# Performance work log

Hardware: AMD Instinct MI355X
Metric: run time of the kernel (lower is better)

Reference implementation:

```python
import jax, jax.numpy as jnp
import numpy as np

R, C, B, E, H = 16, 256, 12, 768, 12  # rows, cols, batch(==heads, see notes), embed, heads
D = E // H
NUM_BUCKETS, MAX_DISTANCE = 32, 50000


def _relative_position_bucket(distances):
    # T5-style log-spaced buckets, matching the torch code (trunc toward zero).
    n = jnp.abs(distances)
    max_exact = NUM_BUCKETS // 2
    is_small = n < max_exact
    nf = jnp.maximum(n.astype(jnp.float32), 1.0)  # guard log(0); masked by is_small
    val_large = max_exact + (
        jnp.log(nf / max_exact) / np.log(MAX_DISTANCE / max_exact) * (NUM_BUCKETS - max_exact - 1)
    ).astype(jnp.int32)
    val_large = jnp.minimum(val_large, NUM_BUCKETS - 1)
    return jnp.where(is_small, n.astype(jnp.int32), val_large)


def setup_inputs() -> dict:
    key = jax.random.key(0)
    ks = jax.random.split(key, 11)
    s = 1.0 / np.sqrt(E)
    x = jax.random.normal(ks[0], (R, C, B, E), jnp.float32)
    distances = jax.random.randint(ks[1], (B, C, C), 0, MAX_DISTANCE, jnp.int32)
    Wq = jax.random.normal(ks[2], (E, E), jnp.float32) * s
    bq = jnp.zeros((E,), jnp.float32)
    Wk = jax.random.normal(ks[3], (E, E), jnp.float32) * s
    bk = jnp.zeros((E,), jnp.float32)
    Wv = jax.random.normal(ks[4], (E, E), jnp.float32) * s
    bv = jnp.zeros((E,), jnp.float32)
    Wo = jax.random.normal(ks[5], (E, E), jnp.float32) * s
    bo = jnp.zeros((E,), jnp.float32)
    rel_bias = jax.random.normal(ks[6], (NUM_BUCKETS, H), jnp.float32) * 0.02
    return dict(x=x, distances=distances, Wq=Wq, bq=bq, Wk=Wk, bk=bk,
                Wv=Wv, bv=bv, Wo=Wo, bo=bo, rel_bias=rel_bias)


def reference(x, distances, Wq, bq, Wk, bk, Wv, bv, Wo, bo, rel_bias):
    scaling = (D ** -0.5) / np.sqrt(R)  # align_scaling: head_dim^-0.5 / sqrt(num_rows)
    q = (x @ Wq.T + bq).reshape(R, C, B, H, D) * scaling
    k = (x @ Wk.T + bk).reshape(R, C, B, H, D)
    # row-aggregated scores: sum over rows r -> (h, n, i, j)
    attn = jnp.einsum('rinhd,rjnhd->hnij', q, k)
    # relative position bias: (n, i, j) -> buckets -> (n, i, j, h) -> (n, h, i, j)
    buckets = _relative_position_bucket(distances)
    bias = jnp.transpose(rel_bias[buckets], (0, 3, 1, 2))
    # NOTE: source adds (n,h,i,j) bias onto (h,n,i,j) scores positionally; valid since B == H.
    attn = attn + bias
    probs = jax.nn.softmax(attn, axis=-1)  # (h, n, i, j)
    v = (x @ Wv.T + bv).reshape(R, C, B, H, D)
    ctx = jnp.einsum('hnij,rjnhd->rinhd', probs, v).reshape(R, C, B, E)
    out = ctx @ Wo.T + bo
    return out, probs
```

## Files before the change

kernel.cpp:

```cpp
#include <hip/hip_runtime.h>
#include <stdint.h>
#include <math.h>

#define R_ 16
#define C_ 256
#define B_ 12
#define E_ 768
#define H_ 12
#define D_ 64
#define TOK (R_*C_*B_)
#define HALF_TOK 24576

#define VT_N_ELEMS 3145728
#define CTX_N_ELEMS 3145728
#define QK_HALF 37748736

typedef __bf16 bf16x8 __attribute__((ext_vector_type(8)));
typedef float floatx4 __attribute__((ext_vector_type(4)));

__device__ __forceinline__ unsigned short f2bf(float f) {
    union { unsigned int i; float f; } v; v.f = f;
    unsigned int i = v.i;
    return (unsigned short)((i + 0x7fffu + ((i >> 16) & 1u)) >> 16);
}
__device__ __forceinline__ bf16x8 cvt8(floatx4 lo, floatx4 hi) {
    bf16x8 r;
    r[0] = (__bf16)lo[0]; r[1] = (__bf16)lo[1]; r[2] = (__bf16)lo[2]; r[3] = (__bf16)lo[3];
    r[4] = (__bf16)hi[0]; r[5] = (__bf16)hi[1]; r[6] = (__bf16)hi[2]; r[7] = (__bf16)hi[3];
    return r;
}
__device__ __forceinline__ void gload16(const unsigned short* g, unsigned short* l) {
    __builtin_amdgcn_global_load_lds(
        (const __attribute__((address_space(1))) unsigned int*)g,
        (__attribute__((address_space(3))) unsigned int*)l, 16, 0, 0);
}

template<int MODE>
__device__ __forceinline__ void gemm_body(const void* __restrict__ Ap,
                                          const void* __restrict__ Btp,
                                          const float* __restrict__ bias,
                                          void* __restrict__ Cout,
                                          int nBase, int rbx, int rby, int rbz,
                                          unsigned short* As, unsigned short* Bs)
{
    constexpr bool AGL = (MODE == 0 || MODE == 1 || MODE == 4);
    constexpr int K = (MODE == 1) ? 1024 : ((MODE == 2) ? 256 : 768);
    constexpr int kIters = K >> 5;
    constexpr int GX = (MODE==0) ? 12 : (MODE==1) ? 2 : (MODE==2) ? 8 : 6;
    constexpr int GY = (MODE==0) ? 192 : (MODE==1) ? 2 : (MODE==2) ? 2 : 32;
    constexpr int GZ = (MODE==0) ? 1 : (MODE==1) ? 144 : (MODE==2) ? 24 : 2;

    const int tid  = threadIdx.x;
    const int wave = tid >> 6, lane = tid & 63;
    const int quad = lane >> 4, l15 = lane & 15;
    const int wr = wave >> 1, wc = wave & 1;

    const int lin = (rbz * GY + rby) * GX + rbx;
    const int tt  = (lin & 7) * ((GX * GY * GZ) >> 3) + (lin >> 3);
    const int bx  = tt % GX;
    const int rem = tt / GX;
    const int by  = rem % GY, bz = rem / GY;
    const int row0 = by * 128, col0 = bx * 128;

    int hIdx = 0, nn = 0, nIdx = 0;
    if (MODE == 1) { hIdx = bz % 12; nIdx = bz / 12; }
    if (MODE == 2) { hIdx = bz % 12; nn = bz / 12; nIdx = nBase + nn; }
    if (MODE == 3 || MODE == 4) { nn = bz; nIdx = nBase + nn; }

    const int rA0 = tid >> 2;
    const int ck  = tid & 3;
    const int sw  = (tid >> 3) & 3;
    const int kko = ((ck ^ sw) << 3);

    const unsigned short* Bt = (const unsigned short*)Btp;
    const unsigned short *gB0, *gB1;
    if (MODE == 1) {
        gB0 = Bt + ((size_t)bz * 256 + col0 + rA0) * 1024 + kko;
        gB1 = Bt + ((size_t)bz * 256 + col0 + rA0 + 64) * 1024 + kko;
    } else if (MODE == 2) {
        gB0 = Bt + (((size_t)nn * 12 + hIdx) * 1024 + col0 + rA0) * 256 + kko;
        gB1 = Bt + (((size_t)nn * 12 + hIdx) * 1024 + col0 + rA0 + 64) * 256 + kko;
    } else {
        gB0 = Bt + (size_t)(col0 + rA0) * 768 + kko;
        gB1 = Bt + (size_t)(col0 + rA0 + 64) * 768 + kko;
    }

    const unsigned short* gA0u = nullptr; const unsigned short* gA1u = nullptr;
    const float* gA0f = nullptr; const float* gA1f = nullptr;
    if (MODE == 0) {
        gA0u = (const unsigned short*)Ap + (size_t)(row0 + rA0) * 768 + kko;
        gA1u = (const unsigned short*)Ap + (size_t)(row0 + rA0 + 64) * 768 + kko;
    } else if (MODE == 1) {
        gA0u = (const unsigned short*)Ap + ((size_t)bz * 256 + row0 + rA0) * 1024 + kko;
        gA1u = (const unsigned short*)Ap + ((size_t)bz * 256 + row0 + rA0 + 64) * 1024 + kko;
    } else if (MODE == 4) {
        gA0u = (const unsigned short*)Ap + (size_t)nn * CTX_N_ELEMS
               + (size_t)(row0 + rA0) * 768 + kko;
        gA1u = (const unsigned short*)Ap + (size_t)nn * CTX_N_ELEMS
               + (size_t)(row0 + rA0 + 64) * 768 + kko;
    } else if (MODE == 3) {
        gA0f = (const float*)Ap + ((size_t)(row0 + rA0) * 12 + nIdx) * 768 + kko;
        gA1f = (const float*)Ap + ((size_t)(row0 + rA0 + 64) * 12 + nIdx) * 768 + kko;
    } else {
        gA0f = (const float*)Ap + ((size_t)(hIdx * 12 + nIdx)) * 65536
               + (size_t)(row0 + rA0) * 256 + kko;
        gA1f = (const float*)Ap + ((size_t)(hIdx * 12 + nIdx)) * 65536
               + (size_t)(row0 + rA0 + 64) * 256 + kko;
    }

    unsigned short* lA0 = As + wave * 512;
    unsigned short* lA1 = As + 2048 + wave * 512;
    unsigned short* lB0 = Bs + wave * 512;
    unsigned short* lB1 = Bs + 2048 + wave * 512;

    const floatx4 zero = {0.f, 0.f, 0.f, 0.f};
    floatx4 acc[4][4];
#pragma unroll
    for (int i = 0; i < 4; ++i)
#pragma unroll
        for (int j = 0; j < 4; ++j) acc[i][j] = zero;

    const int chO = ((quad ^ ((l15 >> 1) & 3)) << 3);

    floatx4 u0l = zero, u0h = zero, u1l = zero, u1h = zero;
    floatx4 p0l = zero, p0h = zero, p1l = zero, p1h = zero;
    if (!AGL) {
        u0l = *(const floatx4*)(gA0f);     u0h = *(const floatx4*)(gA0f + 4);
        u1l = *(const floatx4*)(gA1f);     u1h = *(const floatx4*)(gA1f + 4);
    }

#define GSTEP(KT, UL0, UH0, UL1, UH1, PL0, PH0, PL1, PH1)                         \
    {                                                                              \
        __syncthreads();                                \
        gload16(gB0 + (KT) * 32, lB0);                                             \
        gload16(gB1 + (KT) * 32, lB1);                                             \
        if (AGL) {                                                                 \
            gload16(gA0u + (KT) * 32, lA0);                                        \
            gload16(gA1u + (KT) * 32, lA1);                                        \
        } else {                                                                   \
            *(bf16x8*)(As + tid * 8)        = cvt8(UL0, UH0);                      \
            *(bf16x8*)(As + 2048 + tid * 8) = cvt8(UL1, UH1);                      \
        }                                                                          \
        __syncthreads();                                      \
        if (!AGL && ((KT) + 1 < kIters)) {             \
            PL0 = *(const floatx4*)(gA0f + ((KT) + 1) * 32);                       \
            PH0 = *(const floatx4*)(gA0f + ((KT) + 1) * 32 + 4);                   \
            PL1 = *(const floatx4*)(gA1f + ((KT) + 1) * 32);                       \
            PH1 = *(const floatx4*)(gA1f + ((KT) + 1) * 32 + 4);                   \
        }                                                                          \
        bf16x8 af[4], bfr[4];                                                      \
        _Pragma("unroll")                                                          \
        for (int t = 0; t < 4; ++t) {                                              \
            af[t]  = *(const bf16x8*)(As + (wr * 64 + t * 16 + l15) * 32 + chO);   \
            bfr[t] = *(const bf16x8*)(Bs + (wc * 64 + t * 16 + l15) * 32 + chO);   \
        }                                                                          \
        _Pragma("unroll")                                                          \
        for (int tm = 0; tm < 4; ++tm)                                             \
            _Pragma("unroll")                                                      \
            for (int tn = 0; tn < 4; ++tn)                                         \
                acc[tm][tn] = __builtin_amdgcn_mfma_f32_16x16x32_bf16(             \
                    af[tm], bfr[tn], acc[tm][tn], 0, 0, 0);                        \
    }

    for (int kt = 0; kt < kIters; kt += 2) {
        GSTEP(kt,     u0l, u0h, u1l, u1h, p0l, p0h, p1l, p1h);
        GSTEP(kt + 1, p0l, p0h, p1l, p1h, u0l, u0h, u1l, u1h);
    }
#undef GSTEP

#pragma unroll
    for (int tm = 0; tm < 4; ++tm) {
        const int rbase = row0 + wr * 64 + tm * 16 + quad * 4;
#pragma unroll
        for (int tn = 0; tn < 4; ++tn) {
            const int cc = col0 + wc * 64 + tn * 16 + l15;
#pragma unroll
            for (int rr = 0; rr < 4; ++rr) {
                float vv = acc[tm][tn][rr];
                const int rowg = rbase + rr;
                if (MODE == 0) {
                    const int tg = nBase * HALF_TOK + rowg;
                    const int m = tg / 12, n = tg - m * 12;
                    const int r = m >> 8, i = m & 255;
                    const int sel = cc >= 768 ? 1 : 0;
                    const int ccl = cc - sel * 768;
                    const int h = ccl >> 6, d = ccl & 63;
                    ((unsigned short*)Cout)[(size_t)sel * QK_HALF
                        + ((size_t)(n * 12 + h) * 256 + i) * 1024 + r * 64 + d]
                        = f2bf(vv + bias[cc]);
                } else if (MODE == 1) {
                    ((float*)Cout)[((size_t)(hIdx * 12 + nIdx)) * 65536
                                   + (size_t)rowg * 256 + cc] = vv * 0.03125f;
                } else if (MODE == 2) {
                    ((unsigned short*)Cout)[(size_t)nn * CTX_N_ELEMS
                        + (((size_t)(cc >> 6)) * 256 + rowg) * 768
                        + hIdx * 64 + (cc & 63)] = f2bf(vv);
                } else if (MODE == 3) {
                    ((unsigned short*)Cout)[(size_t)nn * VT_N_ELEMS
                        + (((size_t)(cc >> 6)) * 1024
                           + (rowg >> 8) * 64 + (cc & 63)) * 256
                        + (rowg & 255)] = f2bf(vv + bias[cc]);
                } else {
                    ((float*)Cout)[((size_t)rowg * 12 + nIdx) * 768 + cc] = vv + bias[cc];
                }
            }
        }
    }
}

template<int MODE>
__global__ __launch_bounds__(256)
void gemm_bt(const void* __restrict__ Ap,
             const void* __restrict__ Btp,
             const float* __restrict__ bias,
             void* __restrict__ Cout,
             int nBase)
{
    __shared__ __align__(16) unsigned short As[128 * 32];
    __shared__ __align__(16) unsigned short Bs[128 * 32];
    gemm_body<MODE>(Ap, Btp, bias, Cout, nBase,
                    blockIdx.x, blockIdx.y, blockIdx.z, As, Bs);
}

__global__ __launch_bounds__(256)
void fused_vo(const float* __restrict__ x, const unsigned short* __restrict__ wv,
              const float* __restrict__ bv, unsigned short* __restrict__ vt,
              const unsigned short* __restrict__ ctx,
              const unsigned short* __restrict__ wo,
              const float* __restrict__ bo, float* __restrict__ outp,
              int cV, int cO)
{
    __shared__ __align__(16) unsigned short As[128 * 32];
    __shared__ __align__(16) unsigned short Bs[128 * 32];
    if (blockIdx.z < 2)
        gemm_body<3>(x, wv, bv, vt, cV, blockIdx.x, blockIdx.y, blockIdx.z, As, Bs);
    else
        gemm_body<4>(ctx, wo, bo, outp, cO, blockIdx.x, blockIdx.y,
                     blockIdx.z - 2, As, Bs);
}

__global__ __launch_bounds__(256)
void cvt_bulk(const float* __restrict__ src, unsigned short* __restrict__ dst, int n)
{
    const int i = (blockIdx.x * 256 + threadIdx.x) * 8;
    if (i >= n) return;
    floatx4 a = ((const floatx4*)(src + i))[0];
    floatx4 b = ((const floatx4*)(src + i))[1];
    *(bf16x8*)(dst + i) = cvt8(a, b);
}

__global__ __launch_bounds__(256)
void cvt_weights(const float* __restrict__ Wq, const float* __restrict__ Wk,
                 const float* __restrict__ Wv, const float* __restrict__ Wo,
                 const float* __restrict__ bq, const float* __restrict__ bk,
                 unsigned short* __restrict__ wqk, unsigned short* __restrict__ wvb,
                 unsigned short* __restrict__ wob, float* __restrict__ bqk)
{
    const int gid = blockIdx.x * 256 + threadIdx.x;
    const int W8 = 73728;
    if (gid < 4 * W8) {
        const int sec = gid / W8, off = (gid - sec * W8) * 8;
        const float* src = (sec == 0) ? Wq : (sec == 1) ? Wk : (sec == 2) ? Wv : Wo;
        unsigned short* dst = (sec == 0) ? wqk : (sec == 1) ? (wqk + 589824)
                              : (sec == 2) ? wvb : wob;
        floatx4 a = ((const floatx4*)(src + off))[0];
        floatx4 b = ((const floatx4*)(src + off))[1];
        *(bf16x8*)(dst + off) = cvt8(a, b);
    } else {
        const int b = gid - 4 * W8;
        if (b < 1536) bqk[b] = (b < 768) ? bq[b] : bk[b - 768];
    }
}

__global__ __launch_bounds__(256)
void bucket_kernel(const int* __restrict__ dist, int* __restrict__ buckets)
{
    const int idx = blockIdx.x * 256 + threadIdx.x;
    if (idx >= B_ * C_ * C_) return;
    const int dv = dist[idx];
    const int n = dv < 0 ? -dv : dv;
    int bkt;
    if (n < 16) {
        bkt = n;
    } else {
        const float lg = logf((float)n * 0.0625f);
        const float t  = (lg / 8.047189562170502f) * 15.0f;
        bkt = 16 + (int)t;
        if (bkt > 31) bkt = 31;
    }
    buckets[idx] = bkt;
}

__global__ __launch_bounds__(256)
void softmax_bias(float* __restrict__ probs,
                  const int* __restrict__ buckets,
                  const float* __restrict__ rb)
{
    const int wave = threadIdx.x >> 6, lane = threadIdx.x & 63;
    const int rowid = blockIdx.x * 4 + wave;
    const int p = rowid >> 8;
    const int i = rowid & 255;
    const int a = p / 12, b = p - a * 12;
    float* prow = probs + (size_t)rowid * 256;
    const int* brow = buckets + ((size_t)a * 256 + i) * 256;

    float vals[4];
    float mx = -3.4e38f;
#pragma unroll
    for (int t = 0; t < 4; ++t) {
        const int j = t * 64 + lane;
        vals[t] = prow[j] + rb[brow[j] * 12 + b];
        mx = fmaxf(mx, vals[t]);
    }
#pragma unroll
    for (int off = 32; off > 0; off >>= 1) mx = fmaxf(mx, __shfl_xor(mx, off, 64));
    float sum = 0.f;
#pragma unroll
    for (int t = 0; t < 4; ++t) { vals[t] = expf(vals[t] - mx); sum += vals[t]; }
#pragma unroll
    for (int off = 32; off > 0; off >>= 1) sum += __shfl_xor(sum, off, 64);
    const float inv = 1.f / sum;
#pragma unroll
    for (int t = 0; t < 4; ++t) prow[t * 64 + lane] = vals[t] * inv;
}

extern "C" void kernel_launch(void* const* d_in, const int* in_sizes, int n_in,
                              void* d_out, int out_size, void* d_ws, size_t ws_size,
                              hipStream_t stream)
{
    const float* x    = (const float*)d_in[0];
    const int*   dist = (const int*)d_in[1];
    const float* Wq   = (const float*)d_in[2];
    const float* bq   = (const float*)d_in[3];
    const float* Wk   = (const float*)d_in[4];
    const float* bk   = (const float*)d_in[5];
    const float* Wv   = (const float*)d_in[6];
    const float* bv   = (const float*)d_in[7];
    const float* Wo   = (const float*)d_in[8];
    const float* bo   = (const float*)d_in[9];
    const float* rb   = (const float*)d_in[10];

    float* outp  = (float*)d_out;
    float* probs = (float*)d_out + (size_t)TOK * E_;

    unsigned short* qs   = (unsigned short*)d_out;
    unsigned short* x_bf = (unsigned short*)probs;

    char* ws = (char*)d_ws;
    unsigned short* wo_bf  = (unsigned short*)(ws);
    unsigned short* wv_bf  = (unsigned short*)(ws + 1179648);
    float*          bqk    = (float*)(ws + 2359296);
    unsigned short* wqk_bf = (unsigned short*)(ws + 2365440);
    int*            buckets= (int*)(ws + 4724736);
    unsigned short* vt     = (unsigned short*)(ws + 2365440);
    unsigned short* ctx    = (unsigned short*)(ws + 14948352);

    dim3 blk(256);

    cvt_weights<<<dim3(1158), blk, 0, stream>>>(Wq, Wk, Wv, Wo, bq, bk,
                                                wqk_bf, wv_bf, wo_bf, bqk);
    bucket_kernel<<<dim3(3072), blk, 0, stream>>>(dist, buckets);

    for (int half = 0; half < 2; ++half) {
        cvt_bulk<<<dim3(9216), blk, 0, stream>>>(
            x + (size_t)half * HALF_TOK * 768, x_bf, HALF_TOK * 768);
        gemm_bt<0><<<dim3(12, 192), blk, 0, stream>>>(x_bf, wqk_bf, bqk, qs, half);
    }
    gemm_bt<1><<<dim3(2, 2, 144), blk, 0, stream>>>(
        qs, (unsigned short*)d_out + QK_HALF, nullptr, probs, 0);

    softmax_bias<<<dim3(9216), blk, 0, stream>>>(probs, buckets, rb);

    gemm_bt<3><<<dim3(6, 32, 2), blk, 0, stream>>>(x, wv_bf, bv, vt, 0);
    gemm_bt<2><<<dim3(8, 2, 24), blk, 0, stream>>>(probs, vt, nullptr, ctx, 0);
    for (int k = 1; k < 6; ++k) {
        fused_vo<<<dim3(6, 32, 4), blk, 0, stream>>>(
            x, wv_bf, bv, vt, ctx, wo_bf, bo, outp, 2 * k, 2 * (k - 1));
        gemm_bt<2><<<dim3(8, 2, 24), blk, 0, stream>>>(probs, vt, nullptr, ctx, 2 * k);
    }
    gemm_bt<4><<<dim3(6, 32, 2), blk, 0, stream>>>(ctx, wo_bf, bo, outp, 10);
}
```

Before: 873.3 us.

## Fuse QK score GEMM with bias-add and softmax in one kernel

Replaces the separate QK^T score GEMM and the bias+softmax pass with one kernel. Each 512-thread block computes a full 128x256 row strip of scores and keeps it in registers. It then adds the bucketed relative bias, does the row softmax with shuffles, and writes the probabilities once. This removes one write and one read of the fp32 score matrix and one launch. The cost is a grid of only 288 blocks, single-buffered loads with two barriers per k-step, and 64 accumulator registers per thread, which may lower occupancy and latency hiding.

```diff
diff --git a/kernel.cpp b/kernel.cpp
--- a/kernel.cpp
+++ b/kernel.cpp
@@ -43,12 +43,12 @@
                                           int nBase, int rbx, int rby, int rbz,
                                           unsigned short* As, unsigned short* Bs)
 {
-    constexpr bool AGL = (MODE == 0 || MODE == 1 || MODE == 4);
-    constexpr int K = (MODE == 1) ? 1024 : ((MODE == 2) ? 256 : 768);
+    constexpr bool AGL = (MODE == 0 || MODE == 4);
+    constexpr int K = (MODE == 2) ? 256 : 768;
     constexpr int kIters = K >> 5;
-    constexpr int GX = (MODE==0) ? 12 : (MODE==1) ? 2 : (MODE==2) ? 8 : 6;
-    constexpr int GY = (MODE==0) ? 192 : (MODE==1) ? 2 : (MODE==2) ? 2 : 32;
-    constexpr int GZ = (MODE==0) ? 1 : (MODE==1) ? 144 : (MODE==2) ? 24 : 2;
+    constexpr int GX = (MODE==0) ? 12 : (MODE==2) ? 8 : 6;
+    constexpr int GY = (MODE==0) ? 192 : (MODE==2) ? 2 : 32;
+    constexpr int GZ = (MODE==0) ? 1 : (MODE==2) ? 24 : 2;
 
     const int tid  = threadIdx.x;
     const int wave = tid >> 6, lane = tid & 63;
@@ -63,7 +63,6 @@
     const int row0 = by * 128, col0 = bx * 128;
 
     int hIdx = 0, nn = 0, nIdx = 0;
-    if (MODE == 1) { hIdx = bz % 12; nIdx = bz / 12; }
     if (MODE == 2) { hIdx = bz % 12; nn = bz / 12; nIdx = nBase + nn; }
     if (MODE == 3 || MODE == 4) { nn = bz; nIdx = nBase + nn; }
 
@@ -74,10 +73,7 @@
 
     const unsigned short* Bt = (const unsigned short*)Btp;
     const unsigned short *gB0, *gB1;
-    if (MODE == 1) {
-        gB0 = Bt + ((size_t)bz * 256 + col0 + rA0) * 1024 + kko;
-        gB1 = Bt + ((size_t)bz * 256 + col0 + rA0 + 64) * 1024 + kko;
-    } else if (MODE == 2) {
+    if (MODE == 2) {
         gB0 = Bt + (((size_t)nn * 12 + hIdx) * 1024 + col0 + rA0) * 256 + kko;
         gB1 = Bt + (((size_t)nn * 12 + hIdx) * 1024 + col0 + rA0 + 64) * 256 + kko;
     } else {
@@ -90,9 +86,6 @@
     if (MODE == 0) {
         gA0u = (const unsigned short*)Ap + (size_t)(row0 + rA0) * 768 + kko;
         gA1u = (const unsigned short*)Ap + (size_t)(row0 + rA0 + 64) * 768 + kko;
-    } else if (MODE == 1) {
-        gA0u = (const unsigned short*)Ap + ((size_t)bz * 256 + row0 + rA0) * 1024 + kko;
-        gA1u = (const unsigned short*)Ap + ((size_t)bz * 256 + row0 + rA0 + 64) * 1024 + kko;
     } else if (MODE == 4) {
         gA0u = (const unsigned short*)Ap + (size_t)nn * CTX_N_ELEMS
                + (size_t)(row0 + rA0) * 768 + kko;
@@ -188,9 +181,6 @@
                     ((unsigned short*)Cout)[(size_t)sel * QK_HALF
                         + ((size_t)(n * 12 + h) * 256 + i) * 1024 + r * 64 + d]
                         = f2bf(vv + bias[cc]);
-                } else if (MODE == 1) {
-                    ((float*)Cout)[((size_t)(hIdx * 12 + nIdx)) * 65536
-                                   + (size_t)rowg * 256 + cc] = vv * 0.03125f;
                 } else if (MODE == 2) {
                     ((unsigned short*)Cout)[(size_t)nn * CTX_N_ELEMS
                         + (((size_t)(cc >> 6)) * 256 + rowg) * 768
@@ -239,6 +229,106 @@
                      blockIdx.z - 2, As, Bs);
 }
 
+__global__ __launch_bounds__(512)
+void scores_sm(const unsigned short* __restrict__ q,
+               const unsigned short* __restrict__ k,
+               const int* __restrict__ buckets,
+               const float* __restrict__ rb,
+               float* __restrict__ probs)
+{
+    __shared__ __align__(16) unsigned short As[128 * 32];
+    __shared__ __align__(16) unsigned short Bs[256 * 32];
+
+    const int tid  = threadIdx.x;
+    const int w    = tid >> 6, lane = tid & 63;
+    const int quad = lane >> 4, l15 = lane & 15;
+
+    const int lin = (int)blockIdx.z * 2 + (int)blockIdx.y;
+    const int tt  = (lin & 7) * 36 + (lin >> 3);
+    const int by  = tt % 2, bz = tt / 2;
+    const int row0 = by * 128;
+    const int h = bz % 12, n = bz / 12;
+
+    const int rA0 = tid >> 2;
+    const int ck  = tid & 3;
+    const int sw  = (tid >> 3) & 3;
+    const int kko = ((ck ^ sw) << 3);
+
+    const unsigned short* gA  = q + ((size_t)bz * 256 + row0 + rA0) * 1024 + kko;
+    const unsigned short* gB0 = k + ((size_t)bz * 256 + rA0) * 1024 + kko;
+    const unsigned short* gB1 = k + ((size_t)bz * 256 + rA0 + 128) * 1024 + kko;
+
+    unsigned short* lA  = As + w * 512;
+    unsigned short* lB0 = Bs + w * 512;
+    unsigned short* lB1 = Bs + 4096 + w * 512;
+
+    const floatx4 zero = {0.f, 0.f, 0.f, 0.f};
+    floatx4 acc[16];
+#pragma unroll
+    for (int t = 0; t < 16; ++t) acc[t] = zero;
+
+    const int chO = ((quad ^ ((l15 >> 1) & 3)) << 3);
+
+    for (int kt = 0; kt < 32; ++kt) {
+        __syncthreads();
+        gload16(gA  + kt * 32, lA);
+        gload16(gB0 + kt * 32, lB0);
+        gload16(gB1 + kt * 32, lB1);
+        __syncthreads();
+        const bf16x8 af = *(const bf16x8*)(As + (w * 16 + l15) * 32 + chO);
+#pragma unroll
+        for (int tn = 0; tn < 16; ++tn) {
+            const bf16x8 bfr = *(const bf16x8*)(Bs + (tn * 16 + l15) * 32 + chO);
+            acc[tn] = __builtin_amdgcn_mfma_f32_16x16x32_bf16(af, bfr, acc[tn], 0, 0, 0);
+        }
+    }
+
+    const int i0 = row0 + w * 16 + quad * 4;
+    float mx[4] = {-3.4e38f, -3.4e38f, -3.4e38f, -3.4e38f};
+#pragma unroll
+    for (int tn = 0; tn < 16; ++tn) {
+        const int j = tn * 16 + l15;
+#pragma unroll
+        for (int rr = 0; rr < 4; ++rr) {
+            const int bkt = buckets[((size_t)h * 256 + i0 + rr) * 256 + j];
+            const float s = acc[tn][rr] * 0.03125f + rb[bkt * 12 + n];
+            acc[tn][rr] = s;
+            mx[rr] = fmaxf(mx[rr], s);
+        }
+    }
+#pragma unroll
+    for (int rr = 0; rr < 4; ++rr)
+#pragma unroll
+        for (int off = 1; off < 16; off <<= 1)
+            mx[rr] = fmaxf(mx[rr], __shfl_xor(mx[rr], off, 64));
+    float sm[4] = {0.f, 0.f, 0.f, 0.f};
+#pragma unroll
+    for (int tn = 0; tn < 16; ++tn)
+#pragma unroll
+        for (int rr = 0; rr < 4; ++rr) {
+            const float e = expf(acc[tn][rr] - mx[rr]);
+            acc[tn][rr] = e;
+            sm[rr] += e;
+        }
+#pragma unroll
+    for (int rr = 0; rr < 4; ++rr)
+#pragma unroll
+        for (int off = 1; off < 16; off <<= 1)
+            sm[rr] += __shfl_xor(sm[rr], off, 64);
+    float inv[4];
+#pragma unroll
+    for (int rr = 0; rr < 4; ++rr) inv[rr] = 1.f / sm[rr];
+
+    float* prow = probs + ((size_t)(h * 12 + n)) * 65536;
+#pragma unroll
+    for (int tn = 0; tn < 16; ++tn) {
+        const int j = tn * 16 + l15;
+#pragma unroll
+        for (int rr = 0; rr < 4; ++rr)
+            prow[(size_t)(i0 + rr) * 256 + j] = acc[tn][rr] * inv[rr];
+    }
+}
+
 __global__ __launch_bounds__(256)
 void cvt_bulk(const float* __restrict__ src, unsigned short* __restrict__ dst, int n)
 {
@@ -291,39 +381,6 @@
     buckets[idx] = bkt;
 }
 
-__global__ __launch_bounds__(256)
-void softmax_bias(float* __restrict__ probs,
-                  const int* __restrict__ buckets,
-                  const float* __restrict__ rb)
-{
-    const int wave = threadIdx.x >> 6, lane = threadIdx.x & 63;
-    const int rowid = blockIdx.x * 4 + wave;
-    const int p = rowid >> 8;
-    const int i = rowid & 255;
-    const int a = p / 12, b = p - a * 12;
-    float* prow = probs + (size_t)rowid * 256;
-    const int* brow = buckets + ((size_t)a * 256 + i) * 256;
-
-    float vals[4];
-    float mx = -3.4e38f;
-#pragma unroll
-    for (int t = 0; t < 4; ++t) {
-        const int j = t * 64 + lane;
-        vals[t] = prow[j] + rb[brow[j] * 12 + b];
-        mx = fmaxf(mx, vals[t]);
-    }
-#pragma unroll
-    for (int off = 32; off > 0; off >>= 1) mx = fmaxf(mx, __shfl_xor(mx, off, 64));
-    float sum = 0.f;
-#pragma unroll
-    for (int t = 0; t < 4; ++t) { vals[t] = expf(vals[t] - mx); sum += vals[t]; }
-#pragma unroll
-    for (int off = 32; off > 0; off >>= 1) sum += __shfl_xor(sum, off, 64);
-    const float inv = 1.f / sum;
-#pragma unroll
-    for (int t = 0; t < 4; ++t) prow[t * 64 + lane] = vals[t] * inv;
-}
-
 extern "C" void kernel_launch(void* const* d_in, const int* in_sizes, int n_in,
                               void* d_out, int out_size, void* d_ws, size_t ws_size,
                               hipStream_t stream)
@@ -344,6 +401,7 @@
     float* probs = (float*)d_out + (size_t)TOK * E_;
 
     unsigned short* qs   = (unsigned short*)d_out;
+    unsigned short* ks   = (unsigned short*)d_out + QK_HALF;
     unsigned short* x_bf = (unsigned short*)probs;
 
     char* ws = (char*)d_ws;
@@ -366,10 +424,8 @@
             x + (size_t)half * HALF_TOK * 768, x_bf, HALF_TOK * 768);
         gemm_bt<0><<<dim3(12, 192), blk, 0, stream>>>(x_bf, wqk_bf, bqk, qs, half);
     }
-    gemm_bt<1><<<dim3(2, 2, 144), blk, 0, stream>>>(
-        qs, (unsigned short*)d_out + QK_HALF, nullptr, probs, 0);
-
-    softmax_bias<<<dim3(9216), blk, 0, stream>>>(probs, buckets, rb);
+
+    scores_sm<<<dim3(1, 2, 144), dim3(512), 0, stream>>>(qs, ks, buckets, rb, probs);
 
     gemm_bt<3><<<dim3(6, 32, 2), blk, 0, stream>>>(x, wv_bf, bv, vt, 0);
     gemm_bt<2><<<dim3(8, 2, 24), blk, 0, stream>>>(probs, vt, nullptr, ctx, 0);
```

Result: no change. 872.4 us (-0.1%).
